# Kernel optimization log

Hardware: AMD Instinct MI355X
Metric: run time of the kernel (lower is better)

## Reference

```python
import jax, jax.numpy as jnp
import numpy as np

D_MODEL = 1024
N_HEADS = 16
HEAD_DIM = D_MODEL // N_HEADS
EPS = 1e-6


def _phi(x):
    # elu(x) + 1 feature map
    return jax.nn.elu(x) + 1.0


def setup_inputs() -> dict:
    key = jax.random.key(0)
    ks = jax.random.split(key, 12)
    B, N, M = 4, 4096, 4096
    s = 1.0 / np.sqrt(D_MODEL)
    return {
        "queries": jax.random.normal(ks[0], (B, N, D_MODEL), jnp.float32),
        "keys": jax.random.normal(ks[1], (B, M, D_MODEL), jnp.float32),
        "values": jax.random.normal(ks[2], (B, M, D_MODEL), jnp.float32),
        "wq": jax.random.normal(ks[3], (D_MODEL, D_MODEL), jnp.float32) * s,
        "bq": jax.random.normal(ks[4], (D_MODEL,), jnp.float32) * s,
        "wk": jax.random.normal(ks[5], (D_MODEL, D_MODEL), jnp.float32) * s,
        "bk": jax.random.normal(ks[6], (D_MODEL,), jnp.float32) * s,
        "wv": jax.random.normal(ks[7], (D_MODEL, D_MODEL), jnp.float32) * s,
        "bv": jax.random.normal(ks[8], (D_MODEL,), jnp.float32) * s,
        "wo": jax.random.normal(ks[9], (D_MODEL, D_MODEL), jnp.float32) * s,
        "bo": jax.random.normal(ks[10], (D_MODEL,), jnp.float32) * s,
    }


def reference(queries, keys, values, wq, bq, wk, bk, wv, bv, wo, bo):
    B, N, _ = queries.shape
    M = keys.shape[1]
    H, Dh = N_HEADS, HEAD_DIM
    # projections + head split -> [B, H, seq, Dh]
    q = _phi((queries @ wq.T + bq).reshape(B, N, H, Dh).transpose(0, 2, 1, 3))
    k = _phi((keys @ wk.T + bk).reshape(B, M, H, Dh).transpose(0, 2, 1, 3))
    v = (values @ wv.T + bv).reshape(B, M, H, Dh).transpose(0, 2, 1, 3)
    # kv aggregation: [B,H,Dh,Dh]
    kv = jnp.einsum("bhmd,bhme->bhde", k, v)
    # normalizer: [B,H,Dh]
    z = k.sum(axis=2)
    num = jnp.einsum("bhnd,bhde->bhne", q, kv)
    den = jnp.einsum("bhnd,bhd->bhn", q, z)[..., None] + EPS
    out = (num / den).transpose(0, 2, 1, 3).reshape(B, N, H * Dh)
    return out @ wo.T + bo
```

## Files before the change

kernel.cpp:

```cpp
#include <hip/hip_runtime.h>

#define EPS 1e-6f

typedef __attribute__((ext_vector_type(8))) __bf16 bf16x8;
typedef __attribute__((ext_vector_type(4))) float f32x4;
typedef __attribute__((ext_vector_type(4))) unsigned short us4v;
typedef __attribute__((ext_vector_type(8))) unsigned short us8v;
typedef unsigned short us;

__device__ inline us f2bf(float f) {
  unsigned int u = __builtin_bit_cast(unsigned int, f);
  unsigned int r = (u + 0x7fffu + ((u >> 16) & 1u)) >> 16;
  return (us)r;
}
__device__ inline float bf2f(us s) {
  unsigned int u = ((unsigned int)s) << 16;
  return __builtin_bit_cast(float, u);
}

__device__ inline void gl_lds16(const us* g, us* l) {
  __builtin_amdgcn_global_load_lds(
      (const __attribute__((address_space(1))) unsigned int*)g,
      (__attribute__((address_space(3))) unsigned int*)l, 16, 0, 0);
}

__global__ __launch_bounds__(256) void conv_bf16(const float* __restrict__ s,
                                                 us* __restrict__ d) {
  int idx = blockIdx.x * 256 + threadIdx.x;
  size_t base = (size_t)idx * 8;
  float4 a = *(const float4*)(s + base);
  float4 b = *(const float4*)(s + base + 4);
  us8v o;
  o[0] = f2bf(a.x); o[1] = f2bf(a.y); o[2] = f2bf(a.z); o[3] = f2bf(a.w);
  o[4] = f2bf(b.x); o[5] = f2bf(b.y); o[6] = f2bf(b.z); o[7] = f2bf(b.w);
  *(us8v*)(d + base) = o;
}

template <int MODE>
__global__ __launch_bounds__(512, 2) void proj_gemm(const us* __restrict__ X,
                                                    const us* __restrict__ W,
                                                    const float* __restrict__ bias,
                                                    void* __restrict__ Yv) {
  __shared__ alignas(16) us As[2][256 * 64];
  __shared__ alignas(16) us Bs[2][256 * 64];

  const int t = threadIdx.x;
  const int wave = t >> 6, lane = t & 63;
  const int q4 = lane >> 4, l16 = lane & 15;
  const int wm = wave >> 2, wn = wave & 3;
  const int bid = blockIdx.x;
  const int rowg = (bid & 7) * 8 + (bid >> 5);
  const int colg = (bid >> 3) & 3;
  const int rowBase = rowg << 8;
  const int colBase = colg << 8;

  const int tr = t >> 3;
  const int gsw = ((t & 7) ^ (tr & 7)) * 8;
  const us* Xg = X + (size_t)(rowBase + tr) * 1024 + gsw;
  const us* Wg = W + (size_t)(colBase + tr) * 1024 + gsw;

  const int gx0 = ((0 | q4) ^ (l16 & 7)) * 8;
  const int gx1 = ((4 | q4) ^ (l16 & 7)) * 8;
  const int arow_off = (wm * 128 + l16) * 64;
  const int brow_off = (wn * 64 + l16) * 64;

  f32x4 acc[8][4];
#pragma unroll
  for (int i = 0; i < 8; i++)
#pragma unroll
    for (int j = 0; j < 4; j++) acc[i][j] = (f32x4){0.f, 0.f, 0.f, 0.f};

#define STAGE_A(kt, h)                                                      \
  {                                                                         \
    us* d_ = &As[(kt) & 1][((h) * 128 + wave * 8) * 64];                    \
    const us* s_ = Xg + (size_t)((h) * 128) * 1024 + (kt) * 64;             \
    gl_lds16(s_, d_);                                                       \
    gl_lds16(s_ + (size_t)64 * 1024, d_ + 64 * 64);                         \
  }
#define STAGE_B(kt, h)                                                      \
  {                                                                         \
    us* d_ = &Bs[(kt) & 1][((h) * 128 + wave * 8) * 64];                    \
    const us* s_ = Wg + (size_t)((h) * 128) * 1024 + (kt) * 64;             \
    gl_lds16(s_, d_);                                                       \
    gl_lds16(s_ + (size_t)64 * 1024, d_ + 64 * 64);                         \
  }
#define PH_SYNC_PRE()                                                       \
  asm volatile("s_barrier" ::: "memory");                                   \
  asm volatile("s_waitcnt lgkmcnt(0)" ::: "memory");                        \
  __builtin_amdgcn_sched_barrier(0);                                        \
  __builtin_amdgcn_s_setprio(1);
#define PH_SYNC_POST()                                                      \
  __builtin_amdgcn_s_setprio(0);                                           \
  asm volatile("s_barrier" ::: "memory");
#define MFMA16(J, AF)                                                       \
  _Pragma("unroll") for (int s_i = 0; s_i < 2; ++s_i)                       \
  _Pragma("unroll") for (int ks = 0; ks < 2; ++ks)                          \
  _Pragma("unroll") for (int ni = 0; ni < 4; ++ni)                          \
    acc[2 * (J) + s_i][ni] = __builtin_amdgcn_mfma_f32_16x16x32_bf16(       \
        AF[s_i][ks], bfv[ni][ks], acc[2 * (J) + s_i][ni], 0, 0, 0);

  STAGE_B(0, 0); STAGE_B(0, 1);
  STAGE_A(0, 0); STAGE_A(0, 1);
  STAGE_B(1, 0); STAGE_B(1, 1);
  asm volatile("s_waitcnt vmcnt(4)" ::: "memory");
  asm volatile("s_barrier" ::: "memory");

#pragma unroll 2
  for (int m = 0; m < 16; ++m) {
    const int b = m & 1;
    const us* Ar = &As[b][arow_off];
    const us* Br = &Bs[b][brow_off];
    bf16x8 bfv[4][2];

    {
      bf16x8 af[2][2];
#pragma unroll
      for (int s_i = 0; s_i < 2; ++s_i) {
        af[s_i][0] = *(const bf16x8*)(Ar + (0 + s_i) * 1024 + gx0);
        af[s_i][1] = *(const bf16x8*)(Ar + (0 + s_i) * 1024 + gx1);
      }
#pragma unroll
      for (int ni = 0; ni < 4; ++ni) {
        bfv[ni][0] = *(const bf16x8*)(Br + ni * 1024 + gx0);
        bfv[ni][1] = *(const bf16x8*)(Br + ni * 1024 + gx1);
      }
      if (m < 15) STAGE_A(m + 1, 0);
      PH_SYNC_PRE();
      MFMA16(0, af);
      PH_SYNC_POST();
    }
    {
      bf16x8 af[2][2];
#pragma unroll
      for (int s_i = 0; s_i < 2; ++s_i) {
        af[s_i][0] = *(const bf16x8*)(Ar + (2 + s_i) * 1024 + gx0);
        af[s_i][1] = *(const bf16x8*)(Ar + (2 + s_i) * 1024 + gx1);
      }
      if (m < 15) STAGE_A(m + 1, 1);
      PH_SYNC_PRE();
      MFMA16(1, af);
      PH_SYNC_POST();
    }
    {
      bf16x8 af[2][2];
#pragma unroll
      for (int s_i = 0; s_i < 2; ++s_i) {
        af[s_i][0] = *(const bf16x8*)(Ar + (4 + s_i) * 1024 + gx0);
        af[s_i][1] = *(const bf16x8*)(Ar + (4 + s_i) * 1024 + gx1);
      }
      if (m < 14) STAGE_B(m + 2, 0);
      PH_SYNC_PRE();
      MFMA16(2, af);
      PH_SYNC_POST();
    }
    {
      bf16x8 af[2][2];
#pragma unroll
      for (int s_i = 0; s_i < 2; ++s_i) {
        af[s_i][0] = *(const bf16x8*)(Ar + (6 + s_i) * 1024 + gx0);
        af[s_i][1] = *(const bf16x8*)(Ar + (6 + s_i) * 1024 + gx1);
      }
      if (m < 14) STAGE_B(m + 2, 1);
      asm volatile("s_barrier" ::: "memory");
      asm volatile("s_waitcnt lgkmcnt(0)" ::: "memory");
      __builtin_amdgcn_sched_barrier(0);
      __builtin_amdgcn_s_setprio(1);
      MFMA16(3, af);
      __builtin_amdgcn_s_setprio(0);
      if (m < 14)
        asm volatile("s_waitcnt vmcnt(4)" ::: "memory");
      else
        asm volatile("s_waitcnt vmcnt(0)" ::: "memory");
      asm volatile("s_barrier" ::: "memory");
    }
  }
#undef STAGE_A
#undef STAGE_B
#undef PH_SYNC_PRE
#undef PH_SYNC_POST
#undef MFMA16

#pragma unroll
  for (int j = 0; j < 4; j++) {
    int col = colBase + wn * 64 + j * 16 + l16;
    float bv = bias[col];
#pragma unroll
    for (int i = 0; i < 8; i++) {
      int row0 = rowBase + wm * 128 + i * 16 + q4 * 4;
      if (MODE == 1 || MODE == 2) {
        int bb = row0 >> 12, m0 = row0 & 4095;
        int h = col >> 6, dd = col & 63;
        us4v pk;
#pragma unroll
        for (int r = 0; r < 4; r++) {
          float y = acc[i][j][r] + bv;
          if (MODE == 1) y = (y > 0.f) ? (y + 1.f) : __expf(y);
          pk[r] = f2bf(y);
        }
        *(us4v*)&((us*)Yv)[(((size_t)((bb * 16 + h) * 64 + dd)) << 12) + m0] = pk;
      } else {
#pragma unroll
        for (int r = 0; r < 4; r++) {
          float y = acc[i][j][r] + bv;
          if (MODE == 0) {
            y = (y > 0.f) ? (y + 1.f) : __expf(y);
            ((us*)Yv)[(size_t)(row0 + r) * 1024 + col] = f2bf(y);
          } else {
            ((float*)Yv)[(size_t)(row0 + r) * 1024 + col] = y;
          }
        }
      }
    }
  }
}

__global__ __launch_bounds__(256) void kv_stage1(const us* __restrict__ kt,
                                                 const us* __restrict__ vt,
                                                 float* __restrict__ part,
                                                 float* __restrict__ zpart) {
  __shared__ float red[4][4096];
  __shared__ float zred[4][64][4];

  const int blk = blockIdx.x;
  const int bh = blk >> 2, split = blk & 3;
  const int t = threadIdx.x;
  const int w = t >> 6, lane = t & 63;
  const int q4 = lane >> 4, l16 = lane & 15;
  const us* ktb = kt + (size_t)bh * 64 * 4096;
  const us* vtb = vt + (size_t)bh * 64 * 4096;
  const int mbeg = split * 1024 + w * 256;

  f32x4 acc[4][4];
#pragma unroll
  for (int i = 0; i < 4; i++)
#pragma unroll
    for (int j = 0; j < 4; j++) acc[i][j] = (f32x4){0.f, 0.f, 0.f, 0.f};
  float zacc[4] = {0.f, 0.f, 0.f, 0.f};

  for (int m0 = mbeg; m0 < mbeg + 256; m0 += 32) {
    bf16x8 af[4], bfr[4];
#pragma unroll
    for (int i = 0; i < 4; i++)
      af[i] = *(const bf16x8*)&vtb[(size_t)(i * 16 + l16) * 4096 + m0 + q4 * 8];
#pragma unroll
    for (int j = 0; j < 4; j++) {
      us8v ub = *(const us8v*)&ktb[(size_t)(j * 16 + l16) * 4096 + m0 + q4 * 8];
      bfr[j] = __builtin_bit_cast(bf16x8, ub);
#pragma unroll
      for (int e = 0; e < 8; e++) zacc[j] += bf2f(ub[e]);
    }
#pragma unroll
    for (int i = 0; i < 4; i++)
#pragma unroll
      for (int j = 0; j < 4; j++)
        acc[i][j] = __builtin_amdgcn_mfma_f32_16x16x32_bf16(af[i], bfr[j], acc[i][j], 0, 0, 0);
  }

#pragma unroll
  for (int i = 0; i < 4; i++)
#pragma unroll
    for (int j = 0; j < 4; j++)
#pragma unroll
      for (int r = 0; r < 4; r++)
        red[w][(i * 16 + q4 * 4 + r) * 64 + j * 16 + l16] = acc[i][j][r];
#pragma unroll
  for (int j = 0; j < 4; j++) zred[w][j * 16 + l16][q4] = zacc[j];
  __syncthreads();

  float* pb = part + (size_t)blk * 4096;
#pragma unroll
  for (int i = 0; i < 16; i++) {
    int idx = t + 256 * i;
    pb[idx] = red[0][idx] + red[1][idx] + red[2][idx] + red[3][idx];
  }
  if (t < 64) {
    float s = 0.f;
#pragma unroll
    for (int w2 = 0; w2 < 4; w2++)
#pragma unroll
      for (int q = 0; q < 4; q++) s += zred[w2][t][q];
    zpart[blk * 64 + t] = s;
  }
}

__global__ __launch_bounds__(256) void kv_stage2(const float* __restrict__ part,
                                                 const float* __restrict__ zpart,
                                                 us* __restrict__ kvb,
                                                 float* __restrict__ z) {
  const int bh = blockIdx.x;
  const int t = threadIdx.x;
  const float* p0 = part + (size_t)bh * 4 * 4096;
#pragma unroll
  for (int i = 0; i < 16; i++) {
    int idx = t + 256 * i;
    float s = p0[idx] + p0[4096 + idx] + p0[8192 + idx] + p0[12288 + idx];
    kvb[(size_t)bh * 4096 + idx] = f2bf(s);
  }
  if (t < 64) {
    const float* zp = zpart + (size_t)bh * 4 * 64;
    z[bh * 64 + t] = zp[t] + zp[64 + t] + zp[128 + t] + zp[192 + t];
  }
}

__global__ __launch_bounds__(256) void attn_kernel(const us* __restrict__ q,
                                                   const us* __restrict__ kvb,
                                                   const float* __restrict__ z,
                                                   us* __restrict__ attn) {
  __shared__ alignas(16) us kvs[64 * 72];
  __shared__ float zs[64];
  __shared__ float invden[256];

  const int bid = blockIdx.x;
  const int bh = bid >> 4, nc = bid & 15;
  const int b = bh >> 4, h = bh & 15;
  const int n0 = nc * 256;
  const int t = threadIdx.x;
  const int wave = t >> 6, lane = t & 63;
  const int q4 = lane >> 4, l16 = lane & 15;

#pragma unroll
  for (int i = 0; i < 2; i++) {
    int chunk = t + 256 * i;
    int e = chunk >> 3, d8 = chunk & 7;
    us8v vv = *(const us8v*)&kvb[(size_t)bh * 4096 + chunk * 8];
    *(us8v*)&kvs[e * 72 + d8 * 8] = vv;
  }
  if (t < 64) zs[t] = z[bh * 64 + t];
  __syncthreads();

  {
    const us* qrow = q + ((size_t)(b * 4096 + n0 + t)) * 1024 + h * 64;
    float s = 0.f;
#pragma unroll
    for (int d0 = 0; d0 < 64; d0 += 8) {
      us8v v = *(const us8v*)(qrow + d0);
#pragma unroll
      for (int j = 0; j < 8; j++) s += bf2f(v[j]) * zs[d0 + j];
    }
    invden[t] = 1.0f / (s + EPS);
  }
  __syncthreads();

  f32x4 acc[4][4];
#pragma unroll
  for (int i = 0; i < 4; i++)
#pragma unroll
    for (int j = 0; j < 4; j++) acc[i][j] = (f32x4){0.f, 0.f, 0.f, 0.f};

  const us* qb = q + ((size_t)(b * 4096 + n0 + wave * 64)) * 1024 + h * 64;
#pragma unroll
  for (int ks = 0; ks < 2; ks++) {
    bf16x8 af[4], bfr[4];
#pragma unroll
    for (int i = 0; i < 4; i++)
      af[i] = *(const bf16x8*)(qb + (size_t)(i * 16 + l16) * 1024 + ks * 32 + q4 * 8);
#pragma unroll
    for (int j = 0; j < 4; j++)
      bfr[j] = *(const bf16x8*)&kvs[(j * 16 + l16) * 72 + ks * 32 + q4 * 8];
#pragma unroll
    for (int i = 0; i < 4; i++)
#pragma unroll
      for (int j = 0; j < 4; j++)
        acc[i][j] = __builtin_amdgcn_mfma_f32_16x16x32_bf16(af[i], bfr[j], acc[i][j], 0, 0, 0);
  }

  us* ab = attn + ((size_t)(b * 4096 + n0 + wave * 64)) * 1024 + h * 64;
#pragma unroll
  for (int i = 0; i < 4; i++)
#pragma unroll
    for (int j = 0; j < 4; j++)
#pragma unroll
      for (int r = 0; r < 4; r++) {
        int rowl = i * 16 + q4 * 4 + r;
        int nl = wave * 64 + rowl;
        int e = j * 16 + l16;
        ab[(size_t)rowl * 1024 + e] = f2bf(acc[i][j][r] * invden[nl]);
      }
}

extern "C" void kernel_launch(void* const* d_in, const int* in_sizes, int n_in,
                              void* d_out, int out_size, void* d_ws, size_t ws_size,
                              hipStream_t stream) {
  const float* queries = (const float*)d_in[0];
  const float* keys    = (const float*)d_in[1];
  const float* values  = (const float*)d_in[2];
  const float* wq = (const float*)d_in[3];
  const float* bq = (const float*)d_in[4];
  const float* wk = (const float*)d_in[5];
  const float* bk = (const float*)d_in[6];
  const float* wv = (const float*)d_in[7];
  const float* bv = (const float*)d_in[8];
  const float* wo = (const float*)d_in[9];
  const float* bo = (const float*)d_in[10];

  char* ws = (char*)d_ws;
  const size_t TB = (size_t)16384 * 1024 * 2;
  us* A   = (us*)(ws);
  us* Bb  = (us*)(ws + TB);
  us* Xb  = (us*)(ws + 2 * TB);
  us* wqb = (us*)(ws + 3 * TB);
  us* wkb = wqb + (size_t)1024 * 1024;
  us* wvb = wkb + (size_t)1024 * 1024;
  us* wob = wvb + (size_t)1024 * 1024;
  float* part  = (float*)(wob + (size_t)1024 * 1024);
  float* zpart = part + (size_t)256 * 4096;
  float* z     = zpart + 256 * 64;
  us* kvb      = (us*)(z + 4096);

  const int GRID_IN = 16384 * 1024 / 2048;
  const int GRID_W  = 1024 * 1024 / 2048;

  conv_bf16<<<GRID_W, 256, 0, stream>>>(wq, wqb);
  conv_bf16<<<GRID_W, 256, 0, stream>>>(wk, wkb);
  conv_bf16<<<GRID_W, 256, 0, stream>>>(wv, wvb);
  conv_bf16<<<GRID_W, 256, 0, stream>>>(wo, wob);

  conv_bf16<<<GRID_IN, 256, 0, stream>>>(keys, Xb);
  proj_gemm<1><<<256, 512, 0, stream>>>(Xb, wkb, bk, (void*)A);
  conv_bf16<<<GRID_IN, 256, 0, stream>>>(values, Xb);
  proj_gemm<2><<<256, 512, 0, stream>>>(Xb, wvb, bv, (void*)Bb);
  kv_stage1<<<256, 256, 0, stream>>>(A, Bb, part, zpart);
  kv_stage2<<<64, 256, 0, stream>>>(part, zpart, kvb, z);
  conv_bf16<<<GRID_IN, 256, 0, stream>>>(queries, Bb);
  proj_gemm<0><<<256, 512, 0, stream>>>(Bb, wqb, bq, (void*)A);
  attn_kernel<<<1024, 256, 0, stream>>>(A, kvb, z, A);
  proj_gemm<3><<<256, 512, 0, stream>>>(A, wob, bo, d_out);
}
```

Baseline: 442.2 us.

## Fuse fp32-to-bf16 input conversion into projection GEMM A-tile loads

The projection GEMM now reads fp32 activations straight from global memory into registers, converts them with packed bf16 conversion instructions, and writes them to LDS. This removes the three separate conversion kernels and their full bf16 activation round trips through memory. The four weight conversions are also merged into one launch. In exchange the A operand goes through registers instead of direct global-to-LDS loads, which raises register pressure and doubles the global bytes read per A tile, and the software pipeline's wait counts were retuned by hand.

```diff
diff --git a/kernel.cpp b/kernel.cpp
--- a/kernel.cpp
+++ b/kernel.cpp
@@ -17,6 +17,11 @@
   unsigned int u = ((unsigned int)s) << 16;
   return __builtin_bit_cast(float, u);
 }
+__device__ inline unsigned int cvtpk(float a, float b) {
+  unsigned int d;
+  asm("v_cvt_pk_bf16_f32 %0, %1, %2" : "=v"(d) : "v"(a), "v"(b));
+  return d;
+}
 
 __device__ inline void gl_lds16(const us* g, us* l) {
   __builtin_amdgcn_global_load_lds(
@@ -24,9 +29,19 @@
       (__attribute__((address_space(3))) unsigned int*)l, 16, 0, 0);
 }
 
-__global__ __launch_bounds__(256) void conv_bf16(const float* __restrict__ s,
-                                                 us* __restrict__ d) {
-  int idx = blockIdx.x * 256 + threadIdx.x;
+__global__ __launch_bounds__(256) void conv_w4(const float* __restrict__ wq,
+                                               const float* __restrict__ wk,
+                                               const float* __restrict__ wv,
+                                               const float* __restrict__ wo,
+                                               us* __restrict__ dq,
+                                               us* __restrict__ dk,
+                                               us* __restrict__ dv,
+                                               us* __restrict__ dwo) {
+  int bid = blockIdx.x;
+  int msel = bid >> 9, lb = bid & 511;
+  const float* s = (msel == 0) ? wq : (msel == 1) ? wk : (msel == 2) ? wv : wo;
+  us* d = (msel == 0) ? dq : (msel == 1) ? dk : (msel == 2) ? dv : dwo;
+  int idx = lb * 256 + threadIdx.x;
   size_t base = (size_t)idx * 8;
   float4 a = *(const float4*)(s + base);
   float4 b = *(const float4*)(s + base + 4);
@@ -37,12 +52,16 @@
 }
 
 template <int MODE>
-__global__ __launch_bounds__(512, 2) void proj_gemm(const us* __restrict__ X,
+__global__ __launch_bounds__(512, 2) void proj_gemm(const void* __restrict__ Xv,
                                                     const us* __restrict__ W,
                                                     const float* __restrict__ bias,
                                                     void* __restrict__ Yv) {
+  constexpr bool FP32X = (MODE != 3);
   __shared__ alignas(16) us As[2][256 * 64];
   __shared__ alignas(16) us Bs[2][256 * 64];
+
+  const float* Xf = (const float*)Xv;
+  const us* Xh = (const us*)Xv;
 
   const int t = threadIdx.x;
   const int wave = t >> 6, lane = t & 63;
@@ -55,54 +74,81 @@
   const int colBase = colg << 8;
 
   const int tr = t >> 3;
-  const int gsw = ((t & 7) ^ (tr & 7)) * 8;
-  const us* Xg = X + (size_t)(rowBase + tr) * 1024 + gsw;
-  const us* Wg = W + (size_t)(colBase + tr) * 1024 + gsw;
+  const int g8 = ((t & 7) ^ (tr & 7)) * 8;
+  const us* Wg = W + (size_t)(colBase + tr) * 1024 + g8;
 
   const int gx0 = ((0 | q4) ^ (l16 & 7)) * 8;
   const int gx1 = ((4 | q4) ^ (l16 & 7)) * 8;
   const int arow_off = (wm * 128 + l16) * 64;
   const int brow_off = (wn * 64 + l16) * 64;
 
+  float4 av[2][2][2];
+  uint4 aw[2][2];
+
   f32x4 acc[8][4];
 #pragma unroll
   for (int i = 0; i < 8; i++)
 #pragma unroll
     for (int j = 0; j < 4; j++) acc[i][j] = (f32x4){0.f, 0.f, 0.f, 0.f};
 
-#define STAGE_A(kt, h)                                                      \
-  {                                                                         \
-    us* d_ = &As[(kt) & 1][((h) * 128 + wave * 8) * 64];                    \
-    const us* s_ = Xg + (size_t)((h) * 128) * 1024 + (kt) * 64;             \
-    gl_lds16(s_, d_);                                                       \
-    gl_lds16(s_ + (size_t)64 * 1024, d_ + 64 * 64);                         \
-  }
-#define STAGE_B(kt, h)                                                      \
-  {                                                                         \
-    us* d_ = &Bs[(kt) & 1][((h) * 128 + wave * 8) * 64];                    \
-    const us* s_ = Wg + (size_t)((h) * 128) * 1024 + (kt) * 64;             \
-    gl_lds16(s_, d_);                                                       \
-    gl_lds16(s_ + (size_t)64 * 1024, d_ + 64 * 64);                         \
-  }
-#define PH_SYNC_PRE()                                                       \
-  asm volatile("s_barrier" ::: "memory");                                   \
-  asm volatile("s_waitcnt lgkmcnt(0)" ::: "memory");                        \
-  __builtin_amdgcn_sched_barrier(0);                                        \
+#define ISSUE_A(kt, h)                                                       \
+  if constexpr (FP32X) {                                                     \
+    const float* p_ = Xf + (size_t)(rowBase + (h) * 128 + tr) * 1024 +       \
+                      (kt) * 64 + g8;                                        \
+    av[h][0][0] = *(const float4*)p_;                                        \
+    av[h][0][1] = *(const float4*)(p_ + 4);                                  \
+    av[h][1][0] = *(const float4*)(p_ + 65536);                              \
+    av[h][1][1] = *(const float4*)(p_ + 65536 + 4);                          \
+  } else {                                                                   \
+    const us* p_ = Xh + (size_t)(rowBase + (h) * 128 + tr) * 1024 +          \
+                   (kt) * 64 + g8;                                           \
+    aw[h][0] = *(const uint4*)p_;                                            \
+    aw[h][1] = *(const uint4*)(p_ + 65536);                                  \
+  }
+
+#define WRITE_A(kt, h)                                                       \
+  _Pragma("unroll") for (int r_ = 0; r_ < 2; ++r_) {                         \
+    uint4 o_;                                                                \
+    if constexpr (FP32X) {                                                   \
+      o_.x = cvtpk(av[h][r_][0].x, av[h][r_][0].y);                          \
+      o_.y = cvtpk(av[h][r_][0].z, av[h][r_][0].w);                          \
+      o_.z = cvtpk(av[h][r_][1].x, av[h][r_][1].y);                          \
+      o_.w = cvtpk(av[h][r_][1].z, av[h][r_][1].w);                          \
+    } else {                                                                 \
+      o_ = aw[h][r_];                                                        \
+    }                                                                        \
+    *(uint4*)&As[(kt) & 1][((h) * 128 + wave * 8) * 64 + r_ * 4096 +         \
+                           lane * 8] = o_;                                   \
+  }
+
+#define STAGE_B(kt, h)                                                       \
+  {                                                                          \
+    us* d_ = &Bs[(kt) & 1][((h) * 128 + wave * 8) * 64];                     \
+    const us* s_ = Wg + (size_t)((h) * 128) * 1024 + (kt) * 64;              \
+    gl_lds16(s_, d_);                                                        \
+    gl_lds16(s_ + (size_t)64 * 1024, d_ + 64 * 64);                          \
+  }
+#define PH_SYNC_PRE()                                                        \
+  asm volatile("s_barrier" ::: "memory");                                    \
+  asm volatile("s_waitcnt lgkmcnt(0)" ::: "memory");                         \
+  __builtin_amdgcn_sched_barrier(0);                                         \
   __builtin_amdgcn_s_setprio(1);
-#define PH_SYNC_POST()                                                      \
-  __builtin_amdgcn_s_setprio(0);                                           \
+#define PH_SYNC_POST()                                                       \
+  __builtin_amdgcn_s_setprio(0);                                            \
   asm volatile("s_barrier" ::: "memory");
-#define MFMA16(J, AF)                                                       \
-  _Pragma("unroll") for (int s_i = 0; s_i < 2; ++s_i)                       \
-  _Pragma("unroll") for (int ks = 0; ks < 2; ++ks)                          \
-  _Pragma("unroll") for (int ni = 0; ni < 4; ++ni)                          \
-    acc[2 * (J) + s_i][ni] = __builtin_amdgcn_mfma_f32_16x16x32_bf16(       \
+#define MFMA16(J, AF)                                                        \
+  _Pragma("unroll") for (int s_i = 0; s_i < 2; ++s_i)                        \
+  _Pragma("unroll") for (int ks = 0; ks < 2; ++ks)                           \
+  _Pragma("unroll") for (int ni = 0; ni < 4; ++ni)                           \
+    acc[2 * (J) + s_i][ni] = __builtin_amdgcn_mfma_f32_16x16x32_bf16(        \
         AF[s_i][ks], bfv[ni][ks], acc[2 * (J) + s_i][ni], 0, 0, 0);
 
   STAGE_B(0, 0); STAGE_B(0, 1);
-  STAGE_A(0, 0); STAGE_A(0, 1);
+  ISSUE_A(0, 0); ISSUE_A(0, 1);
   STAGE_B(1, 0); STAGE_B(1, 1);
   asm volatile("s_waitcnt vmcnt(4)" ::: "memory");
+  WRITE_A(0, 0); WRITE_A(0, 1);
+  asm volatile("s_waitcnt lgkmcnt(0)" ::: "memory");
   asm volatile("s_barrier" ::: "memory");
 
 #pragma unroll 2
@@ -124,7 +170,7 @@
         bfv[ni][0] = *(const bf16x8*)(Br + ni * 1024 + gx0);
         bfv[ni][1] = *(const bf16x8*)(Br + ni * 1024 + gx1);
       }
-      if (m < 15) STAGE_A(m + 1, 0);
+      if (m < 15) { ISSUE_A(m + 1, 0); }
       PH_SYNC_PRE();
       MFMA16(0, af);
       PH_SYNC_POST();
@@ -136,7 +182,7 @@
         af[s_i][0] = *(const bf16x8*)(Ar + (2 + s_i) * 1024 + gx0);
         af[s_i][1] = *(const bf16x8*)(Ar + (2 + s_i) * 1024 + gx1);
       }
-      if (m < 15) STAGE_A(m + 1, 1);
+      if (m < 15) { ISSUE_A(m + 1, 1); }
       PH_SYNC_PRE();
       MFMA16(1, af);
       PH_SYNC_POST();
@@ -147,6 +193,13 @@
       for (int s_i = 0; s_i < 2; ++s_i) {
         af[s_i][0] = *(const bf16x8*)(Ar + (4 + s_i) * 1024 + gx0);
         af[s_i][1] = *(const bf16x8*)(Ar + (4 + s_i) * 1024 + gx1);
+      }
+      if (m < 15) {
+        if constexpr (FP32X)
+          asm volatile("s_waitcnt vmcnt(4)" ::: "memory");
+        else
+          asm volatile("s_waitcnt vmcnt(2)" ::: "memory");
+        WRITE_A(m + 1, 0);
       }
       if (m < 14) STAGE_B(m + 2, 0);
       PH_SYNC_PRE();
@@ -160,21 +213,21 @@
         af[s_i][0] = *(const bf16x8*)(Ar + (6 + s_i) * 1024 + gx0);
         af[s_i][1] = *(const bf16x8*)(Ar + (6 + s_i) * 1024 + gx1);
       }
+      if (m < 15) {
+        if (m < 14)
+          asm volatile("s_waitcnt vmcnt(2)" ::: "memory");
+        else
+          asm volatile("s_waitcnt vmcnt(0)" ::: "memory");
+        WRITE_A(m + 1, 1);
+      }
       if (m < 14) STAGE_B(m + 2, 1);
-      asm volatile("s_barrier" ::: "memory");
-      asm volatile("s_waitcnt lgkmcnt(0)" ::: "memory");
-      __builtin_amdgcn_sched_barrier(0);
-      __builtin_amdgcn_s_setprio(1);
+      PH_SYNC_PRE();
       MFMA16(3, af);
-      __builtin_amdgcn_s_setprio(0);
-      if (m < 14)
-        asm volatile("s_waitcnt vmcnt(4)" ::: "memory");
-      else
-        asm volatile("s_waitcnt vmcnt(0)" ::: "memory");
-      asm volatile("s_barrier" ::: "memory");
-    }
-  }
-#undef STAGE_A
+      PH_SYNC_POST();
+    }
+  }
+#undef ISSUE_A
+#undef WRITE_A
 #undef STAGE_B
 #undef PH_SYNC_PRE
 #undef PH_SYNC_POST
@@ -397,7 +450,6 @@
   const size_t TB = (size_t)16384 * 1024 * 2;
   us* A   = (us*)(ws);
   us* Bb  = (us*)(ws + TB);
-  us* Xb  = (us*)(ws + 2 * TB);
   us* wqb = (us*)(ws + 3 * TB);
   us* wkb = wqb + (size_t)1024 * 1024;
   us* wvb = wkb + (size_t)1024 * 1024;
@@ -407,22 +459,13 @@
   float* z     = zpart + 256 * 64;
   us* kvb      = (us*)(z + 4096);
 
-  const int GRID_IN = 16384 * 1024 / 2048;
-  const int GRID_W  = 1024 * 1024 / 2048;
-
-  conv_bf16<<<GRID_W, 256, 0, stream>>>(wq, wqb);
-  conv_bf16<<<GRID_W, 256, 0, stream>>>(wk, wkb);
-  conv_bf16<<<GRID_W, 256, 0, stream>>>(wv, wvb);
-  conv_bf16<<<GRID_W, 256, 0, stream>>>(wo, wob);
-
-  conv_bf16<<<GRID_IN, 256, 0, stream>>>(keys, Xb);
-  proj_gemm<1><<<256, 512, 0, stream>>>(Xb, wkb, bk, (void*)A);
-  conv_bf16<<<GRID_IN, 256, 0, stream>>>(values, Xb);
-  proj_gemm<2><<<256, 512, 0, stream>>>(Xb, wvb, bv, (void*)Bb);
+  conv_w4<<<2048, 256, 0, stream>>>(wq, wk, wv, wo, wqb, wkb, wvb, wob);
+
+  proj_gemm<1><<<256, 512, 0, stream>>>((const void*)keys, wkb, bk, (void*)A);
+  proj_gemm<2><<<256, 512, 0, stream>>>((const void*)values, wvb, bv, (void*)Bb);
   kv_stage1<<<256, 256, 0, stream>>>(A, Bb, part, zpart);
   kv_stage2<<<64, 256, 0, stream>>>(part, zpart, kvb, z);
-  conv_bf16<<<GRID_IN, 256, 0, stream>>>(queries, Bb);
-  proj_gemm<0><<<256, 512, 0, stream>>>(Bb, wqb, bq, (void*)A);
+  proj_gemm<0><<<256, 512, 0, stream>>>((const void*)queries, wqb, bq, (void*)A);
   attn_kernel<<<1024, 256, 0, stream>>>(A, kvb, z, A);
-  proj_gemm<3><<<256, 512, 0, stream>>>(A, wob, bo, d_out);
-}
+  proj_gemm<3><<<256, 512, 0, stream>>>((const void*)A, wob, bo, d_out);
+}
```

Measured after the change: 436.3 us. About the same (-1.3%).
